# Optimization experiments

Hardware: AMD Instinct MI355X
Metric: run time of the kernel (lower is better)

## Reference

```python
import jax, jax.numpy as jnp
import numpy as np

SYM_LIST = jnp.array([0, 1, 2, 3])  # init kwarg sym_list


def setup_inputs() -> dict:
    key = jax.random.key(0)
    k1, k2, k3, k4 = jax.random.split(key, 4)
    bs, n = 16, 2048
    target = jax.random.normal(k1, (bs, n, 3), dtype=jnp.float32)
    model_points = jax.random.normal(k2, (bs, n, 3), dtype=jnp.float32)
    idx = jax.random.randint(k3, (bs, 1), 0, 8)
    H = jax.random.normal(k4, (bs, 4, 4), dtype=jnp.float32)
    return {"target": target, "model_points": model_points, "idx": idx, "H": H}


def reference(target, model_points, idx, H):
    # base = H[:, :3, :3]^T per batch; pred = model_points @ base + t
    base = jnp.swapaxes(H[:, :3, :3], 1, 2)            # [bs, 3, 3]
    t = H[:, :3, 3][:, None, :]                        # [bs, 1, 3]
    tf = jnp.einsum('bnd,bde->bne', model_points, base) + t  # [bs, N, 3]

    # Squared pairwise distances (argmin-equivalent to L2 norm used in knn()).
    # d2[b, q, r] = ||tf[b,q] - target[b,r]||^2
    d2 = (jnp.sum(tf * tf, axis=-1)[:, :, None]
          + jnp.sum(target * target, axis=-1)[:, None, :]
          - 2.0 * jnp.einsum('bqd,brd->bqr', tf, target))  # [bs, N, N]
    inds = jnp.argmin(d2, axis=2)                      # [bs, N] nearest target per query
    gathered = jnp.take_along_axis(target, inds[:, :, None], axis=1)  # [bs, N, 3]

    # Only symmetric objects (idx in sym_list) get the NN-rearranged target.
    is_sym = jnp.isin(idx[:, 0], SYM_LIST)[:, None, None]  # [bs, 1, 1]
    tgt = jnp.where(is_sym, gathered, target)

    # dis = mean_n ||tf - tgt||_2, per batch element
    dis = jnp.mean(jnp.linalg.norm(tf - tgt, axis=2), axis=1)  # [bs]
    return dis
```

## Files before the change

### kernel.cpp

```cpp
#include <hip/hip_runtime.h>

#define N 2048
#define BS 16
#define QG 512
#define NQG (N / QG)
#define TS 64
#define NTS (N / TS)
#define WAVES 4
#define TPB (WAVES * 64)
#define TPW (TS / WAVES)
#define QPL 8


__global__ __launch_bounds__(TPB, 4) void addsloss_k1(
    const float* __restrict__ target,
    const float* __restrict__ mp,
    const int* __restrict__ idx,
    const float* __restrict__ H,
    float* __restrict__ wsmin)
{
    __shared__ float4 tlds[TS];
    __shared__ float  pmin[WAVES][QG];

    const int bid  = blockIdx.x;
    const int b    = bid >> 7;
    const int rem  = bid & 127;
    const int qg   = rem >> 5;
    const int ts   = rem & 31;
    const int tid  = threadIdx.x;
    const int wave = tid >> 6;
    const int lane = tid & 63;

    const int  cls = idx[b];
    const bool sym = (cls >= 0) && (cls <= 3);
    if (!sym) return;

    const float* tb = target + (size_t)b * N * 3;
    const float* mb = mp     + (size_t)b * N * 3;
    const float* hb = H      + b * 16;

    if (tid < TS) {
        const int t = ts * TS + tid;
        const float x = tb[t * 3 + 0];
        const float y = tb[t * 3 + 1];
        const float z = tb[t * 3 + 2];
        tlds[tid] = make_float4(x, y, z, x * x + y * y + z * z);
    }

    float ngx[QPL], ngy[QPL], ngz[QPL];
    #pragma unroll
    for (int qi = 0; qi < QPL; ++qi) {
        const int q = qg * QG + qi * 64 + lane;
        const float m0 = mb[q * 3 + 0];
        const float m1 = mb[q * 3 + 1];
        const float m2 = mb[q * 3 + 2];
        ngx[qi] = -2.0f * (hb[0] * m0 + hb[1]  * m1 + hb[2]  * m2 + hb[3]);
        ngy[qi] = -2.0f * (hb[4] * m0 + hb[5]  * m1 + hb[6]  * m2 + hb[7]);
        ngz[qi] = -2.0f * (hb[8] * m0 + hb[9]  * m1 + hb[10] * m2 + hb[11]);
    }

    __syncthreads();

    const float4* t4 = &tlds[wave * TPW];

    float acc[QPL][4];
    #pragma unroll
    for (int qi = 0; qi < QPL; ++qi)
        #pragma unroll
        for (int ti = 0; ti < 4; ++ti) acc[qi][ti] = 3.4e38f;

    #pragma unroll
    for (int j = 0; j < TPW / 4; ++j) {
        const float4 T0 = t4[j * 4 + 0];
        const float4 T1 = t4[j * 4 + 1];
        const float4 T2 = t4[j * 4 + 2];
        const float4 T3 = t4[j * 4 + 3];
        #pragma unroll
        for (int qi = 0; qi < QPL; ++qi) {
            float h;
            h = T0.w; h = fmaf(ngx[qi], T0.x, h); h = fmaf(ngy[qi], T0.y, h);
            h = fmaf(ngz[qi], T0.z, h); acc[qi][0] = fminf(acc[qi][0], h);
            h = T1.w; h = fmaf(ngx[qi], T1.x, h); h = fmaf(ngy[qi], T1.y, h);
            h = fmaf(ngz[qi], T1.z, h); acc[qi][1] = fminf(acc[qi][1], h);
            h = T2.w; h = fmaf(ngx[qi], T2.x, h); h = fmaf(ngy[qi], T2.y, h);
            h = fmaf(ngz[qi], T2.z, h); acc[qi][2] = fminf(acc[qi][2], h);
            h = T3.w; h = fmaf(ngx[qi], T3.x, h); h = fmaf(ngy[qi], T3.y, h);
            h = fmaf(ngz[qi], T3.z, h); acc[qi][3] = fminf(acc[qi][3], h);
        }
    }

    #pragma unroll
    for (int qi = 0; qi < QPL; ++qi)
        pmin[wave][qi * 64 + lane] =
            fminf(fminf(acc[qi][0], acc[qi][1]), fminf(acc[qi][2], acc[qi][3]));
    __syncthreads();

    float* wrow = wsmin + ((size_t)(b * NTS + ts)) * N + qg * QG;
    #pragma unroll
    for (int k = 0; k < QG / TPB; ++k) {
        const int i = k * TPB + tid;
        wrow[i] = fminf(fminf(pmin[0][i], pmin[1][i]),
                        fminf(pmin[2][i], pmin[3][i]));
    }
}

__global__ __launch_bounds__(256) void addsloss_k2(
    const float* __restrict__ target,
    const float* __restrict__ mp,
    const int* __restrict__ idx,
    const float* __restrict__ H,
    const float* __restrict__ wsmin,
    float* __restrict__ ws2)
{
    __shared__ float ps[4];
    const int bid  = blockIdx.x;
    const int b    = bid >> 3;
    const int part = bid & 7;
    const int tid  = threadIdx.x;
    const int wave = tid >> 6;
    const int lane = tid & 63;
    const int q    = part * 256 + tid;

    const int  cls = idx[b];
    const bool sym = (cls >= 0) && (cls <= 3);

    const float* tb = target + (size_t)b * N * 3;
    const float* mb = mp     + (size_t)b * N * 3;
    const float* hb = H      + b * 16;

    const float m0 = mb[q * 3 + 0];
    const float m1 = mb[q * 3 + 1];
    const float m2 = mb[q * 3 + 2];
    const float fx = hb[0] * m0 + hb[1]  * m1 + hb[2]  * m2 + hb[3];
    const float fy = hb[4] * m0 + hb[5]  * m1 + hb[6]  * m2 + hb[7];
    const float fz = hb[8] * m0 + hb[9]  * m1 + hb[10] * m2 + hb[11];

    float d;
    if (sym) {
        float m = 3.4e38f;
        #pragma unroll
        for (int t = 0; t < NTS; ++t)
            m = fminf(m, wsmin[((size_t)(b * NTS + t)) * N + q]);
        const float c = fx * fx + fy * fy + fz * fz;
        d = sqrtf(fmaxf(0.0f, c + m));
    } else {
        const float dx = fx - tb[q * 3 + 0];
        const float dy = fy - tb[q * 3 + 1];
        const float dz = fz - tb[q * 3 + 2];
        d = sqrtf(dx * dx + dy * dy + dz * dz);
    }

    #pragma unroll
    for (int off = 32; off > 0; off >>= 1) d += __shfl_down(d, off);
    if (lane == 0) ps[wave] = d;
    __syncthreads();
    if (tid == 0) ws2[bid] = ps[0] + ps[1] + ps[2] + ps[3];
}

__global__ __launch_bounds__(64) void addsloss_k3(
    const float* __restrict__ ws2, float* __restrict__ out)
{
    const int b = threadIdx.x;
    if (b < BS) {
        float s = 0.0f;
        #pragma unroll
        for (int p = 0; p < 8; ++p) s += ws2[b * 8 + p];
        out[b] = s * (1.0f / (float)N);
    }
}

extern "C" void kernel_launch(void* const* d_in, const int* in_sizes, int n_in,
                              void* d_out, int out_size, void* d_ws, size_t ws_size,
                              hipStream_t stream) {
    const float* target = (const float*)d_in[0];
    const float* mp     = (const float*)d_in[1];
    const int*   idx    = (const int*)  d_in[2];
    const float* H      = (const float*)d_in[3];
    float*       out    = (float*)d_out;
    float*       wsmin  = (float*)d_ws;
    float*       ws2    = wsmin + (size_t)BS * NTS * N;

    addsloss_k1<<<BS * NQG * NTS, TPB, 0, stream>>>(target, mp, idx, H, wsmin);
    addsloss_k2<<<BS * 8, 256, 0, stream>>>(target, mp, idx, H, wsmin, ws2);
    addsloss_k3<<<1, 64, 0, stream>>>(ws2, out);
}
```

Before: 15.78 us.

## Fuse three kernels into one with full-target LDS tile and atomic last-block reduction

Replaces the three-kernel pipeline (partial min per target tile, cross-tile min and sqrt, final mean) with a single kernel. Each block holds a batch's whole target set in LDS and handles 128 queries over 8 waves. A per-batch atomic counter lets the last-finishing block produce the mean. This drops the large intermediate min buffer and two launches, but each block now loads all 2048 targets (32KB LDS), parallelism drops to 256 blocks with only 2 queries per lane, and a memset is added.

```diff
diff --git a/kernel.cpp b/kernel.cpp
--- a/kernel.cpp
+++ b/kernel.cpp
@@ -2,124 +2,32 @@
 
 #define N 2048
 #define BS 16
-#define QG 512
-#define NQG (N / QG)
-#define TS 64
-#define NTS (N / TS)
-#define WAVES 4
+#define NQG 16
+#define QG 128
+#define WAVES 8
 #define TPB (WAVES * 64)
-#define TPW (TS / WAVES)
-#define QPL 8
+#define TPW (N / WAVES)
+#define QPL 2
 
-
-__global__ __launch_bounds__(TPB, 4) void addsloss_k1(
+__global__ __launch_bounds__(TPB) void addsloss_fused(
     const float* __restrict__ target,
     const float* __restrict__ mp,
     const int* __restrict__ idx,
     const float* __restrict__ H,
-    float* __restrict__ wsmin)
+    float* __restrict__ partial,
+    unsigned int* __restrict__ cnt,
+    float* __restrict__ out)
 {
-    __shared__ float4 tlds[TS];
+    __shared__ float4 tlds[N];
     __shared__ float  pmin[WAVES][QG];
+    __shared__ float  dsum[QG];
 
     const int bid  = blockIdx.x;
-    const int b    = bid >> 7;
-    const int rem  = bid & 127;
-    const int qg   = rem >> 5;
-    const int ts   = rem & 31;
+    const int b    = bid >> 4;
+    const int qg   = bid & 15;
     const int tid  = threadIdx.x;
     const int wave = tid >> 6;
     const int lane = tid & 63;
-
-    const int  cls = idx[b];
-    const bool sym = (cls >= 0) && (cls <= 3);
-    if (!sym) return;
-
-    const float* tb = target + (size_t)b * N * 3;
-    const float* mb = mp     + (size_t)b * N * 3;
-    const float* hb = H      + b * 16;
-
-    if (tid < TS) {
-        const int t = ts * TS + tid;
-        const float x = tb[t * 3 + 0];
-        const float y = tb[t * 3 + 1];
-        const float z = tb[t * 3 + 2];
-        tlds[tid] = make_float4(x, y, z, x * x + y * y + z * z);
-    }
-
-    float ngx[QPL], ngy[QPL], ngz[QPL];
-    #pragma unroll
-    for (int qi = 0; qi < QPL; ++qi) {
-        const int q = qg * QG + qi * 64 + lane;
-        const float m0 = mb[q * 3 + 0];
-        const float m1 = mb[q * 3 + 1];
-        const float m2 = mb[q * 3 + 2];
-        ngx[qi] = -2.0f * (hb[0] * m0 + hb[1]  * m1 + hb[2]  * m2 + hb[3]);
-        ngy[qi] = -2.0f * (hb[4] * m0 + hb[5]  * m1 + hb[6]  * m2 + hb[7]);
-        ngz[qi] = -2.0f * (hb[8] * m0 + hb[9]  * m1 + hb[10] * m2 + hb[11]);
-    }
-
-    __syncthreads();
-
-    const float4* t4 = &tlds[wave * TPW];
-
-    float acc[QPL][4];
-    #pragma unroll
-    for (int qi = 0; qi < QPL; ++qi)
-        #pragma unroll
-        for (int ti = 0; ti < 4; ++ti) acc[qi][ti] = 3.4e38f;
-
-    #pragma unroll
-    for (int j = 0; j < TPW / 4; ++j) {
-        const float4 T0 = t4[j * 4 + 0];
-        const float4 T1 = t4[j * 4 + 1];
-        const float4 T2 = t4[j * 4 + 2];
-        const float4 T3 = t4[j * 4 + 3];
-        #pragma unroll
-        for (int qi = 0; qi < QPL; ++qi) {
-            float h;
-            h = T0.w; h = fmaf(ngx[qi], T0.x, h); h = fmaf(ngy[qi], T0.y, h);
-            h = fmaf(ngz[qi], T0.z, h); acc[qi][0] = fminf(acc[qi][0], h);
-            h = T1.w; h = fmaf(ngx[qi], T1.x, h); h = fmaf(ngy[qi], T1.y, h);
-            h = fmaf(ngz[qi], T1.z, h); acc[qi][1] = fminf(acc[qi][1], h);
-            h = T2.w; h = fmaf(ngx[qi], T2.x, h); h = fmaf(ngy[qi], T2.y, h);
-            h = fmaf(ngz[qi], T2.z, h); acc[qi][2] = fminf(acc[qi][2], h);
-            h = T3.w; h = fmaf(ngx[qi], T3.x, h); h = fmaf(ngy[qi], T3.y, h);
-            h = fmaf(ngz[qi], T3.z, h); acc[qi][3] = fminf(acc[qi][3], h);
-        }
-    }
-
-    #pragma unroll
-    for (int qi = 0; qi < QPL; ++qi)
-        pmin[wave][qi * 64 + lane] =
-            fminf(fminf(acc[qi][0], acc[qi][1]), fminf(acc[qi][2], acc[qi][3]));
-    __syncthreads();
-
-    float* wrow = wsmin + ((size_t)(b * NTS + ts)) * N + qg * QG;
-    #pragma unroll
-    for (int k = 0; k < QG / TPB; ++k) {
-        const int i = k * TPB + tid;
-        wrow[i] = fminf(fminf(pmin[0][i], pmin[1][i]),
-                        fminf(pmin[2][i], pmin[3][i]));
-    }
-}
-
-__global__ __launch_bounds__(256) void addsloss_k2(
-    const float* __restrict__ target,
-    const float* __restrict__ mp,
-    const int* __restrict__ idx,
-    const float* __restrict__ H,
-    const float* __restrict__ wsmin,
-    float* __restrict__ ws2)
-{
-    __shared__ float ps[4];
-    const int bid  = blockIdx.x;
-    const int b    = bid >> 3;
-    const int part = bid & 7;
-    const int tid  = threadIdx.x;
-    const int wave = tid >> 6;
-    const int lane = tid & 63;
-    const int q    = part * 256 + tid;
 
     const int  cls = idx[b];
     const bool sym = (cls >= 0) && (cls <= 3);
@@ -128,44 +36,105 @@
     const float* mb = mp     + (size_t)b * N * 3;
     const float* hb = H      + b * 16;
 
-    const float m0 = mb[q * 3 + 0];
-    const float m1 = mb[q * 3 + 1];
-    const float m2 = mb[q * 3 + 2];
-    const float fx = hb[0] * m0 + hb[1]  * m1 + hb[2]  * m2 + hb[3];
-    const float fy = hb[4] * m0 + hb[5]  * m1 + hb[6]  * m2 + hb[7];
-    const float fz = hb[8] * m0 + hb[9]  * m1 + hb[10] * m2 + hb[11];
+    if (sym) {
+        for (int i = tid; i < N; i += TPB) {
+            const float x = tb[i * 3 + 0];
+            const float y = tb[i * 3 + 1];
+            const float z = tb[i * 3 + 2];
+            tlds[i] = make_float4(x, y, z, x * x + y * y + z * z);
+        }
 
-    float d;
-    if (sym) {
-        float m = 3.4e38f;
+        float ngx[QPL], ngy[QPL], ngz[QPL];
         #pragma unroll
-        for (int t = 0; t < NTS; ++t)
-            m = fminf(m, wsmin[((size_t)(b * NTS + t)) * N + q]);
-        const float c = fx * fx + fy * fy + fz * fz;
-        d = sqrtf(fmaxf(0.0f, c + m));
+        for (int qi = 0; qi < QPL; ++qi) {
+            const int q = qg * QG + qi * 64 + lane;
+            const float m0 = mb[q * 3 + 0];
+            const float m1 = mb[q * 3 + 1];
+            const float m2 = mb[q * 3 + 2];
+            ngx[qi] = -2.0f * (hb[0] * m0 + hb[1]  * m1 + hb[2]  * m2 + hb[3]);
+            ngy[qi] = -2.0f * (hb[4] * m0 + hb[5]  * m1 + hb[6]  * m2 + hb[7]);
+            ngz[qi] = -2.0f * (hb[8] * m0 + hb[9]  * m1 + hb[10] * m2 + hb[11]);
+        }
+
+        __syncthreads();
+
+        const float4* t4 = &tlds[wave * TPW];
+
+        float acc[QPL][4];
+        #pragma unroll
+        for (int qi = 0; qi < QPL; ++qi)
+            #pragma unroll
+            for (int ti = 0; ti < 4; ++ti) acc[qi][ti] = 3.4e38f;
+
+        #pragma unroll 2
+        for (int j = 0; j < TPW / 4; ++j) {
+            const float4 T0 = t4[j * 4 + 0];
+            const float4 T1 = t4[j * 4 + 1];
+            const float4 T2 = t4[j * 4 + 2];
+            const float4 T3 = t4[j * 4 + 3];
+            #pragma unroll
+            for (int qi = 0; qi < QPL; ++qi) {
+                float h;
+                h = T0.w; h = fmaf(ngx[qi], T0.x, h); h = fmaf(ngy[qi], T0.y, h);
+                h = fmaf(ngz[qi], T0.z, h); acc[qi][0] = fminf(acc[qi][0], h);
+                h = T1.w; h = fmaf(ngx[qi], T1.x, h); h = fmaf(ngy[qi], T1.y, h);
+                h = fmaf(ngz[qi], T1.z, h); acc[qi][1] = fminf(acc[qi][1], h);
+                h = T2.w; h = fmaf(ngx[qi], T2.x, h); h = fmaf(ngy[qi], T2.y, h);
+                h = fmaf(ngz[qi], T2.z, h); acc[qi][2] = fminf(acc[qi][2], h);
+                h = T3.w; h = fmaf(ngx[qi], T3.x, h); h = fmaf(ngy[qi], T3.y, h);
+                h = fmaf(ngz[qi], T3.z, h); acc[qi][3] = fminf(acc[qi][3], h);
+            }
+        }
+
+        #pragma unroll
+        for (int qi = 0; qi < QPL; ++qi)
+            pmin[wave][qi * 64 + lane] =
+                fminf(fminf(acc[qi][0], acc[qi][1]), fminf(acc[qi][2], acc[qi][3]));
+        __syncthreads();
+
+        if (tid < QG) {
+            float m = pmin[0][tid];
+            #pragma unroll
+            for (int w = 1; w < WAVES; ++w) m = fminf(m, pmin[w][tid]);
+            const int qi = tid >> 6;
+            const float c = 0.25f * (ngx[qi] * ngx[qi] + ngy[qi] * ngy[qi]
+                                     + ngz[qi] * ngz[qi]);
+            dsum[tid] = sqrtf(fmaxf(0.0f, c + m));
+        }
     } else {
-        const float dx = fx - tb[q * 3 + 0];
-        const float dy = fy - tb[q * 3 + 1];
-        const float dz = fz - tb[q * 3 + 2];
-        d = sqrtf(dx * dx + dy * dy + dz * dz);
+        if (tid < QG) {
+            const int q = qg * QG + tid;
+            const float m0 = mb[q * 3 + 0];
+            const float m1 = mb[q * 3 + 1];
+            const float m2 = mb[q * 3 + 2];
+            const float fx = hb[0] * m0 + hb[1]  * m1 + hb[2]  * m2 + hb[3];
+            const float fy = hb[4] * m0 + hb[5]  * m1 + hb[6]  * m2 + hb[7];
+            const float fz = hb[8] * m0 + hb[9]  * m1 + hb[10] * m2 + hb[11];
+            const float dx = fx - tb[q * 3 + 0];
+            const float dy = fy - tb[q * 3 + 1];
+            const float dz = fz - tb[q * 3 + 2];
+            dsum[tid] = sqrtf(dx * dx + dy * dy + dz * dz);
+        }
     }
 
-    #pragma unroll
-    for (int off = 32; off > 0; off >>= 1) d += __shfl_down(d, off);
-    if (lane == 0) ps[wave] = d;
     __syncthreads();
-    if (tid == 0) ws2[bid] = ps[0] + ps[1] + ps[2] + ps[3];
-}
 
-__global__ __launch_bounds__(64) void addsloss_k3(
-    const float* __restrict__ ws2, float* __restrict__ out)
-{
-    const int b = threadIdx.x;
-    if (b < BS) {
-        float s = 0.0f;
+    if (wave == 0) {
+        float s = dsum[lane] + dsum[lane + 64];
         #pragma unroll
-        for (int p = 0; p < 8; ++p) s += ws2[b * 8 + p];
-        out[b] = s * (1.0f / (float)N);
+        for (int off = 32; off > 0; off >>= 1) s += __shfl_down(s, off);
+        if (lane == 0) {
+            partial[bid] = s;
+            __threadfence();
+            const unsigned int old = atomicAdd(&cnt[b], 1u);
+            if (old == NQG - 1) {
+                __threadfence();
+                float tot = 0.0f;
+                #pragma unroll
+                for (int p = 0; p < NQG; ++p) tot += partial[b * NQG + p];
+                out[b] = tot * (1.0f / (float)N);
+            }
+        }
     }
 }
 
@@ -177,10 +146,10 @@
     const int*   idx    = (const int*)  d_in[2];
     const float* H      = (const float*)d_in[3];
     float*       out    = (float*)d_out;
-    float*       wsmin  = (float*)d_ws;
-    float*       ws2    = wsmin + (size_t)BS * NTS * N;
+    float*        partial = (float*)d_ws;
+    unsigned int* cntp    = (unsigned int*)((char*)d_ws + 1024);
 
-    addsloss_k1<<<BS * NQG * NTS, TPB, 0, stream>>>(target, mp, idx, H, wsmin);
-    addsloss_k2<<<BS * 8, 256, 0, stream>>>(target, mp, idx, H, wsmin, ws2);
-    addsloss_k3<<<1, 64, 0, stream>>>(ws2, out);
+    hipMemsetAsync((char*)d_ws + 1024, 0, 64, stream);
+    addsloss_fused<<<BS * NQG, TPB, 0, stream>>>(target, mp, idx, H,
+                                                 partial, cntp, out);
 }
```

Measured after the change: 21.97 us. +39.2%, slower.
